# Performance work log

Hardware: AMD Instinct MI355X
Metric: run time of the kernel (lower is better)

The kernel has to match this reference:

```python
import jax, jax.numpy as jnp
import numpy as np

PRE_HEIGHT = 96
PRE_WIDTH = 128


def setup_inputs() -> dict:
    key = jax.random.key(0)
    B, K, H, W = 32, 64, 96, 128
    x = jax.random.normal(key, (B, K, H, W), dtype=jnp.float32)
    return {"combined_hm_preds": x, "batch_size": B, "num_of_kp": K}


def reference(combined_hm_preds, batch_size, num_of_kp):
    B, K, H, W = combined_hm_preds.shape
    # nn.Softmax() with no dim on a 4D tensor -> softmax over dim=1 (channels)
    map_val_all = jax.nn.softmax(combined_hm_preds, axis=1)
    # zeta[b,k] = sum over spatial of the channel-softmaxed map
    get_zeta = map_val_all.sum(axis=(2, 3))  # [B, K]
    js = jnp.arange(W, dtype=map_val_all.dtype)
    iis = jnp.arange(H, dtype=map_val_all.dtype)
    # per-channel weighted coordinate sums
    Sx = jnp.einsum('bkij,j->bk', map_val_all, js)  # [B, K]
    Sy = jnp.einsum('bkij,i->bk', map_val_all, iis)  # [B, K]
    # faithful to the original: accumulators are never reset across k or b,
    # so each keypoint uses the inclusive cumulative sum in flattened (b,k) order
    cum_x = jnp.cumsum(Sx.reshape(-1)).reshape(B, K)
    cum_y = jnp.cumsum(Sy.reshape(-1)).reshape(B, K)
    kx = jnp.round(cum_x / get_zeta)
    ky = jnp.round(cum_y / get_zeta)
    # out-of-range clamp to the image center, as in the original
    kx = jnp.where((kx > PRE_WIDTH) | (kx < 0), PRE_WIDTH * 0.5, kx)
    ky = jnp.where((ky > PRE_HEIGHT) | (ky < 0), PRE_HEIGHT * 0.5, ky)
    keypoint = jnp.stack([kx, ky], axis=-1)  # [B, K, 2]
    return (map_val_all, keypoint, get_zeta)
```

## Files before the change

### kernel.cpp

```cpp
#include <hip/hip_runtime.h>
#include <math.h>

#define BB 32
#define KK 64
#define HH 96
#define WW 128
#define HW (HH*WW)
#define MAP_SIZE (BB*KK*HW)
#define NBK (BB*KK)

__global__ __launch_bounds__(256) void den_k(const float* __restrict__ x,
                                             float* __restrict__ inv_den) {
    int gid = blockIdx.x * 256 + threadIdx.x;
    int b   = gid / (HW / 4);
    int p4  = gid - b * (HW / 4);
    const float4* xp = (const float4*)(x + (size_t)b * KK * HW) + p4;

    float4 s = {0.f, 0.f, 0.f, 0.f};
    #pragma unroll
    for (int k = 0; k < KK; ++k) {
        float4 v = xp[(size_t)k * (HW / 4)];
        s.x += __expf(v.x);
        s.y += __expf(v.y);
        s.z += __expf(v.z);
        s.w += __expf(v.w);
    }
    float4 r = {1.f / s.x, 1.f / s.y, 1.f / s.z, 1.f / s.w};
    ((float4*)inv_den)[gid] = r;
}

__global__ __launch_bounds__(256) void map_reduce_k(const float* __restrict__ x,
                                                    const float* __restrict__ inv_den,
                                                    float* __restrict__ out,
                                                    float* __restrict__ zeta,
                                                    double* __restrict__ sxyz) {
    int bk = blockIdx.x;
    int b  = bk >> 6;
    const float4* xp = (const float4*)(x        + (size_t)bk * HW);
    const float4* ip = (const float4*)(inv_den  + (size_t)b  * HW);
    float4*       op = (float4*)      (out      + (size_t)bk * HW);
    int t = threadIdx.x;

    double z = 0.0, sx = 0.0, sy = 0.0;
    #pragma unroll
    for (int it = 0; it < 12; ++it) {
        int idx = it * 256 + t;
        float4 v   = xp[idx];
        float4 inv = ip[idx];
        float4 m;
        m.x = __expf(v.x) * inv.x;
        m.y = __expf(v.y) * inv.y;
        m.z = __expf(v.z) * inv.z;
        m.w = __expf(v.w) * inv.w;
        op[idx] = m;
        int j0 = (idx & 31) * 4;
        int i  = idx >> 5;
        float qs = m.x + m.y + m.z + m.w;
        float qx = m.x * (float)j0 + m.y * (float)(j0 + 1)
                 + m.z * (float)(j0 + 2) + m.w * (float)(j0 + 3);
        z  += (double)qs;
        sx += (double)qx;
        sy += (double)i * (double)qs;
    }
    for (int off = 32; off > 0; off >>= 1) {
        z  += __shfl_down(z,  off, 64);
        sx += __shfl_down(sx, off, 64);
        sy += __shfl_down(sy, off, 64);
    }
    __shared__ double sz[4], ssx[4], ssy[4];
    int lane = t & 63, wid = t >> 6;
    if (lane == 0) { sz[wid] = z; ssx[wid] = sx; ssy[wid] = sy; }
    __syncthreads();
    if (t == 0) {
        double Z  = sz[0]  + sz[1]  + sz[2]  + sz[3];
        double SX = ssx[0] + ssx[1] + ssx[2] + ssx[3];
        double SY = ssy[0] + ssy[1] + ssy[2] + ssy[3];
        sxyz[bk * 3 + 0] = SX;
        sxyz[bk * 3 + 1] = SY;
        sxyz[bk * 3 + 2] = Z;
        zeta[bk] = (float)Z;
    }
}

__global__ __launch_bounds__(256) void keypoint_k(const double* __restrict__ sxyz,
                                                  float* __restrict__ kp) {
    const int PT = NBK / 256;
    int t = threadIdx.x;
    int lane = t & 63, wid = t >> 6;

    double vx[PT], vy[PT];
    double cx = 0.0, cy = 0.0;
    #pragma unroll
    for (int e = 0; e < PT; ++e) {
        int idx = t * PT + e;
        cx += sxyz[idx * 3 + 0]; vx[e] = cx;
        cy += sxyz[idx * 3 + 1]; vy[e] = cy;
    }
    double tx = cx, ty = cy;
    for (int off = 1; off < 64; off <<= 1) {
        double ax = __shfl_up(tx, off, 64);
        double ay = __shfl_up(ty, off, 64);
        if (lane >= off) { tx += ax; ty += ay; }
    }
    __shared__ double wxs[4], wys[4];
    if (lane == 63) { wxs[wid] = tx; wys[wid] = ty; }
    __syncthreads();
    double offx = tx - cx, offy = ty - cy;
    for (int w2 = 0; w2 < wid; ++w2) { offx += wxs[w2]; offy += wys[w2]; }

    #pragma unroll
    for (int e = 0; e < PT; ++e) {
        int idx = t * PT + e;
        double zz = sxyz[idx * 3 + 2];
        double kx = rint((vx[e] + offx) / zz);
        double ky = rint((vy[e] + offy) / zz);
        float fkx = (float)kx, fky = (float)ky;
        if (fkx > 128.0f || fkx < 0.0f) fkx = 64.0f;
        if (fky > 96.0f  || fky < 0.0f) fky = 48.0f;
        kp[idx * 2 + 0] = fkx;
        kp[idx * 2 + 1] = fky;
    }
}

extern "C" void kernel_launch(void* const* d_in, const int* in_sizes, int n_in,
                              void* d_out, int out_size, void* d_ws, size_t ws_size,
                              hipStream_t stream) {
    const float* x = (const float*)d_in[0];
    float* out  = (float*)d_out;
    float* map  = out;
    float* kp   = out + MAP_SIZE;
    float* zeta = out + MAP_SIZE + NBK * 2;

    double* sxyz = (double*)d_ws;
    float*  inv  = (float*)((char*)d_ws + NBK * 3 * sizeof(double) + 256);

    den_k       <<< (BB * HW / 4) / 256, 256, 0, stream >>> (x, inv);
    map_reduce_k<<< NBK,                 256, 0, stream >>> (x, inv, map, zeta, sxyz);
    keypoint_k  <<< 1,                   256, 0, stream >>> (sxyz, kp);
}
```

Measured before the change: 198.0 us.

## Fuse softmax denominator and map reduction into one LDS-tiled kernel with atomics

Merges the denominator and normalize/reduce kernels so each block loads a 256-pixel tile across all 64 channels once, caches exponentials in shared memory, writes the softmax map, and reduces per-channel sums. Partial zeta/Sx/Sy sums are accumulated with double atomics into a zeroed workspace, and zeta is written in the keypoint kernel. This removes the second read of the input and the inverse-denominator buffer, in exchange for large LDS use limiting occupancy, scalar loads, and atomic contention.

```diff
diff --git a/kernel.cpp b/kernel.cpp
--- a/kernel.cpp
+++ b/kernel.cpp
@@ -8,82 +8,67 @@
 #define HW (HH*WW)
 #define MAP_SIZE (BB*KK*HW)
 #define NBK (BB*KK)
+#define NT  (HW/256)
 
-__global__ __launch_bounds__(256) void den_k(const float* __restrict__ x,
-                                             float* __restrict__ inv_den) {
-    int gid = blockIdx.x * 256 + threadIdx.x;
-    int b   = gid / (HW / 4);
-    int p4  = gid - b * (HW / 4);
-    const float4* xp = (const float4*)(x + (size_t)b * KK * HW) + p4;
+__global__ __launch_bounds__(256) void fused_k(const float* __restrict__ x,
+                                               float* __restrict__ out,
+                                               double* __restrict__ sxyz) {
+    __shared__ float  sm[KK][257];
+    __shared__ float  dinv[256];
+    __shared__ double pz[4][64], px[4][64], py[4][64];
 
-    float4 s = {0.f, 0.f, 0.f, 0.f};
+    int blk  = blockIdx.x;
+    int b    = blk / NT;
+    int tile = blk - b * NT;
+    int t    = threadIdx.x;
+    size_t base = (size_t)b * KK * HW + (size_t)tile * 256 + t;
+
+    float den = 0.f;
     #pragma unroll
     for (int k = 0; k < KK; ++k) {
-        float4 v = xp[(size_t)k * (HW / 4)];
-        s.x += __expf(v.x);
-        s.y += __expf(v.y);
-        s.z += __expf(v.z);
-        s.w += __expf(v.w);
+        float e = __expf(x[base + (size_t)k * HW]);
+        sm[k][t] = e;
+        den += e;
     }
-    float4 r = {1.f / s.x, 1.f / s.y, 1.f / s.z, 1.f / s.w};
-    ((float4*)inv_den)[gid] = r;
-}
+    float inv = 1.f / den;
+    dinv[t] = inv;
 
-__global__ __launch_bounds__(256) void map_reduce_k(const float* __restrict__ x,
-                                                    const float* __restrict__ inv_den,
-                                                    float* __restrict__ out,
-                                                    float* __restrict__ zeta,
-                                                    double* __restrict__ sxyz) {
-    int bk = blockIdx.x;
-    int b  = bk >> 6;
-    const float4* xp = (const float4*)(x        + (size_t)bk * HW);
-    const float4* ip = (const float4*)(inv_den  + (size_t)b  * HW);
-    float4*       op = (float4*)      (out      + (size_t)bk * HW);
-    int t = threadIdx.x;
+    #pragma unroll
+    for (int k = 0; k < KK; ++k) {
+        out[base + (size_t)k * HW] = sm[k][t] * inv;
+    }
 
+    __syncthreads();
+
+    int k = t & 63, chunk = t >> 6;
+    int p0 = chunk * 64;
     double z = 0.0, sx = 0.0, sy = 0.0;
     #pragma unroll
-    for (int it = 0; it < 12; ++it) {
-        int idx = it * 256 + t;
-        float4 v   = xp[idx];
-        float4 inv = ip[idx];
-        float4 m;
-        m.x = __expf(v.x) * inv.x;
-        m.y = __expf(v.y) * inv.y;
-        m.z = __expf(v.z) * inv.z;
-        m.w = __expf(v.w) * inv.w;
-        op[idx] = m;
-        int j0 = (idx & 31) * 4;
-        int i  = idx >> 5;
-        float qs = m.x + m.y + m.z + m.w;
-        float qx = m.x * (float)j0 + m.y * (float)(j0 + 1)
-                 + m.z * (float)(j0 + 2) + m.w * (float)(j0 + 3);
-        z  += (double)qs;
-        sx += (double)qx;
-        sy += (double)i * (double)qs;
+    for (int j = 0; j < 64; ++j) {
+        int p = p0 + j;
+        double m = (double)(sm[k][p] * dinv[p]);
+        int g = tile * 256 + p;
+        z  += m;
+        sx += m * (double)(g & (WW - 1));
+        sy += m * (double)(g >> 7);
     }
-    for (int off = 32; off > 0; off >>= 1) {
-        z  += __shfl_down(z,  off, 64);
-        sx += __shfl_down(sx, off, 64);
-        sy += __shfl_down(sy, off, 64);
-    }
-    __shared__ double sz[4], ssx[4], ssy[4];
-    int lane = t & 63, wid = t >> 6;
-    if (lane == 0) { sz[wid] = z; ssx[wid] = sx; ssy[wid] = sy; }
+    pz[chunk][k] = z; px[chunk][k] = sx; py[chunk][k] = sy;
     __syncthreads();
-    if (t == 0) {
-        double Z  = sz[0]  + sz[1]  + sz[2]  + sz[3];
-        double SX = ssx[0] + ssx[1] + ssx[2] + ssx[3];
-        double SY = ssy[0] + ssy[1] + ssy[2] + ssy[3];
-        sxyz[bk * 3 + 0] = SX;
-        sxyz[bk * 3 + 1] = SY;
-        sxyz[bk * 3 + 2] = Z;
-        zeta[bk] = (float)Z;
+
+    if (t < 64) {
+        double Z  = pz[0][t] + pz[1][t] + pz[2][t] + pz[3][t];
+        double SX = px[0][t] + px[1][t] + px[2][t] + px[3][t];
+        double SY = py[0][t] + py[1][t] + py[2][t] + py[3][t];
+        int bk = b * KK + t;
+        atomicAdd(&sxyz[bk * 3 + 0], SX);
+        atomicAdd(&sxyz[bk * 3 + 1], SY);
+        atomicAdd(&sxyz[bk * 3 + 2], Z);
     }
 }
 
 __global__ __launch_bounds__(256) void keypoint_k(const double* __restrict__ sxyz,
-                                                  float* __restrict__ kp) {
+                                                  float* __restrict__ kp,
+                                                  float* __restrict__ zeta) {
     const int PT = NBK / 256;
     int t = threadIdx.x;
     int lane = t & 63, wid = t >> 6;
@@ -119,6 +104,7 @@
         if (fky > 96.0f  || fky < 0.0f) fky = 48.0f;
         kp[idx * 2 + 0] = fkx;
         kp[idx * 2 + 1] = fky;
+        zeta[idx] = (float)zz;
     }
 }
 
@@ -130,11 +116,9 @@
     float* map  = out;
     float* kp   = out + MAP_SIZE;
     float* zeta = out + MAP_SIZE + NBK * 2;
+    double* sxyz = (double*)d_ws;
 
-    double* sxyz = (double*)d_ws;
-    float*  inv  = (float*)((char*)d_ws + NBK * 3 * sizeof(double) + 256);
-
-    den_k       <<< (BB * HW / 4) / 256, 256, 0, stream >>> (x, inv);
-    map_reduce_k<<< NBK,                 256, 0, stream >>> (x, inv, map, zeta, sxyz);
-    keypoint_k  <<< 1,                   256, 0, stream >>> (sxyz, kp);
+    hipMemsetAsync(d_ws, 0, (size_t)NBK * 3 * sizeof(double), stream);
+    fused_k   <<< BB * NT, 256, 0, stream >>> (x, map, sxyz);
+    keypoint_k<<< 1,       256, 0, stream >>> (sxyz, kp, zeta);
 }
```

Result: faster. 189.0 us (-4.5%).
